# Kernel tuning notes

Hardware: AMD Instinct MI355X
Metric: run time of the kernel (lower is better)

The kernel has to match this reference:

```python
import jax, jax.numpy as jnp
import numpy as np

B, N, K, CIN, COUT = 2, 8192, 16, 64, 64


def setup_inputs() -> dict:
    key = jax.random.key(0)
    ks = jax.random.split(key, 12)
    w = lambda k, shape: jax.random.normal(k, shape, jnp.float32) * 0.02
    return dict(
        pos=jax.random.normal(ks[0], (B, N, 3), jnp.float32),
        features=jax.random.normal(ks[1], (B, N, CIN), jnp.float32),
        emb_w=w(ks[2], (CIN, COUT)), emb_b=jnp.zeros((COUT,), jnp.float32),
        wq=w(ks[3], (COUT, COUT)), wk=w(ks[4], (COUT, COUT)), wv=w(ks[5], (COUT, COUT)),
        pe_w1=w(ks[6], (3, COUT)), pe_b1=jnp.zeros((COUT,), jnp.float32),
        pe_w2=w(ks[7], (COUT, COUT)), pe_b2=jnp.zeros((COUT,), jnp.float32),
        at_w1=w(ks[8], (COUT, COUT)), at_b1=jnp.zeros((COUT,), jnp.float32),
        at_w2=w(ks[9], (COUT, COUT)), at_b2=jnp.zeros((COUT,), jnp.float32),
        out_w=w(ks[10], (COUT, CIN)), out_b=jnp.zeros((CIN,), jnp.float32),
    )


def _gather(x, idx):
    # x: [B, N, C], idx: [B, N, K] -> [B, N, K, C]
    return jax.vmap(lambda xb, ib: xb[ib])(x, idx)


def reference(pos, features, emb_w, emb_b, wq, wk, wv,
              pe_w1, pe_b1, pe_w2, pe_b2,
              at_w1, at_b1, at_w2, at_b2, out_w, out_b):
    # KNN: squared pairwise distances, take k smallest (includes self)
    sq = jnp.sum(pos * pos, axis=-1)                                  # [B, N]
    d2 = sq[:, :, None] + sq[:, None, :] - 2.0 * jnp.einsum('bnd,bmd->bnm', pos, pos)
    _, knn_idx = jax.lax.top_k(-d2, K)                                # [B, N, K]

    # recenter_groups: neighbor positions relative to query point
    grouped_pos = _gather(pos, knn_idx) - pos[:, :, None, :]          # [B, N, K, 3]

    x = features @ emb_w + emb_b                                      # [B, N, COUT]
    q = x @ wq                                                        # [B, N, COUT]
    k = _gather(x @ wk, knn_idx)                                      # [B, N, K, COUT]
    v = _gather(x @ wv, knn_idx)                                      # [B, N, K, COUT]

    # mlp_posenc: Linear(3,C) -> ReLU -> Linear(C,C)
    posenc = jax.nn.relu(grouped_pos @ pe_w1 + pe_b1) @ pe_w2 + pe_b2  # [B, N, K, COUT]

    # mlp_attn on (q - k + posenc), softmax over neighbor axis (dim=-2)
    h = q[:, :, None, :] - k + posenc
    attn = jax.nn.relu(h @ at_w1 + at_b1) @ at_w2 + at_b2
    attn = jax.nn.softmax(attn / np.float32(np.sqrt(COUT)), axis=-2)

    result = jnp.einsum('bmnf,bmnf->bmf', attn, v + posenc)           # [B, N, COUT]
    return result @ out_w + out_b + features                          # [B, N, CIN]
```

## Files before the change

### kernel.cpp

```cpp
#include <hip/hip_runtime.h>
#include <hip/hip_bf16.h>

#define BB 2
#define NN 8192
#define SPL 16
#define CAND (NN/SPL)
#define NPTS (BB*NN)

#define POS4_OFF 0u
#define WBUF_OFF 65536u
#define PART_OFF 99328u
#define QB_OFF   99328u
#define KVB_OFF  (QB_OFF + 1048576u)
#define IDX_OFF  4293632u
#define WT_OFF   (IDX_OFF + 262144u)

#define W_EMB 0
#define W_Q   4096
#define W_K   8192
#define W_V   12288
#define W_PE2 16384
#define W_AT1 20480
#define W_AT2 24576
#define W_OUT 28672
#define W_PE1 32768
#define B_EMB 32960
#define B_PE1 33024
#define B_PE2 33088
#define B_AT1 33152
#define B_AT2 33216
#define B_OUT 33280

typedef __attribute__((ext_vector_type(8))) short bf16x8;
typedef __attribute__((ext_vector_type(4))) float f32x4;

__device__ __forceinline__ unsigned umn(unsigned a, unsigned b) {
#if __has_builtin(__builtin_elementwise_min)
  return __builtin_elementwise_min(a, b);
#else
  return a < b ? a : b;
#endif
}
__device__ __forceinline__ unsigned umx(unsigned a, unsigned b) {
#if __has_builtin(__builtin_elementwise_max)
  return __builtin_elementwise_max(a, b);
#else
  return a < b ? b : a;
#endif
}

__device__ inline unsigned short f2bf(float x) {
  __hip_bfloat16 b = __float2bfloat16(x);
  return *(unsigned short*)&b;
}

#define HCOL(c, j) ((((((c) >> 3) + (j)) & 7) << 3) | ((c) & 7))

__global__ __launch_bounds__(256) void k0_stage(
    const float* __restrict__ pos,
    const float* __restrict__ emb_w, const float* __restrict__ emb_b,
    const float* __restrict__ wq, const float* __restrict__ wk,
    const float* __restrict__ wv,
    const float* __restrict__ pe_w1, const float* __restrict__ pe_b1,
    const float* __restrict__ pe_w2, const float* __restrict__ pe_b2,
    const float* __restrict__ at_w1, const float* __restrict__ at_b1,
    const float* __restrict__ at_w2, const float* __restrict__ at_b2,
    const float* __restrict__ out_w, const float* __restrict__ out_b,
    float* __restrict__ ws)
{
  int t = blockIdx.x * 256 + threadIdx.x;
  if (t < NPTS) {
    float x = pos[t * 3 + 0], y = pos[t * 3 + 1], z = pos[t * 3 + 2];
    float* o = ws + POS4_OFF + t * 4;
    o[0] = x; o[1] = y; o[2] = z;
    o[3] = fmaf(x, x, fmaf(y, y, z * z));
    return;
  }
  t -= NPTS;
  float* wbuf = ws + WBUF_OFF;
  if (t < 32768) {
    const float* s;
    switch (t >> 12) {
      case 0: s = emb_w; break;
      case 1: s = wq;    break;
      case 2: s = wk;    break;
      case 3: s = wv;    break;
      case 4: s = pe_w2; break;
      case 5: s = at_w1; break;
      case 6: s = at_w2; break;
      default: s = out_w; break;
    }
    wbuf[t] = s[t & 4095];
    return;
  }
  t -= 32768;
  if (t < 192) { wbuf[W_PE1 + t] = pe_w1[t]; return; }
  t -= 192;
  if (t < 384) {
    const float* s;
    switch (t >> 6) {
      case 0: s = emb_b; break;
      case 1: s = pe_b1; break;
      case 2: s = pe_b2; break;
      case 3: s = at_b1; break;
      case 4: s = at_b2; break;
      default: s = out_b; break;
    }
    wbuf[B_EMB + t] = s[t & 63];
    return;
  }
  t -= 384;
  if (t < 16384) {
    unsigned short* wt = (unsigned short*)(ws + WT_OFF);
    const float* s;
    switch (t >> 12) {
      case 0: s = pe_w2; break;
      case 1: s = at_w1; break;
      case 2: s = at_w2; break;
      default: s = out_w; break;
    }
    int idx = t & 4095, f = idx >> 6, c = idx & 63;
    wt[t] = f2bf(s[c * 64 + f]);
  }
}

__global__ __launch_bounds__(256) void k1_knn(const float* __restrict__ pos4,
                                              unsigned* __restrict__ part)
{
  const int tid = threadIdx.x;
  const int g = blockIdx.x * 256 + tid;
  const int s = blockIdx.y;
  const int bu = __builtin_amdgcn_readfirstlane(g >> 13);
  const float4* __restrict__ allp = (const float4*)pos4;
  const float4 q = allp[g];
  const float qx2 = -2.f * q.x, qy2 = -2.f * q.y, qz2 = -2.f * q.z;
  const float sqq = q.w + 1e-5f;
  const float4* __restrict__ cand = allp + (bu * NN + s * CAND);
  unsigned m[16];
#pragma unroll
  for (int i = 0; i < 16; i++) m[i] = 0xFFFFFFFFu;
  const unsigned jb = (unsigned)(s * CAND);

  constexpr int OE[63][2] = {
    {0,1},{2,3},{4,5},{6,7},{8,9},{10,11},{12,13},{14,15},
    {0,2},{1,3},{4,6},{5,7},{8,10},{9,11},{12,14},{13,15},
    {1,2},{5,6},{9,10},{13,14},
    {0,4},{1,5},{2,6},{3,7},{8,12},{9,13},{10,14},{11,15},
    {2,4},{3,5},{10,12},{11,13},
    {1,2},{3,4},{5,6},{9,10},{11,12},{13,14},
    {0,8},{1,9},{2,10},{3,11},{4,12},{5,13},{6,14},{7,15},
    {4,8},{5,9},{6,10},{7,11},
    {2,4},{3,5},{6,8},{7,9},{10,12},{11,13},
    {1,2},{3,4},{5,6},{7,8},{9,10},{11,12},{13,14}
  };

  for (int j0 = 0; j0 < CAND; j0 += 16) {
    unsigned b[16];
#pragma unroll
    for (int i = 0; i < 16; i++) {
      float4 cp = cand[j0 + i];
      float d2 = fmaf(cp.x, qx2, fmaf(cp.y, qy2, fmaf(cp.z, qz2, cp.w + sqq)));
      b[i] = (__float_as_uint(d2) & 0xFFFFE000u) | (jb + (unsigned)(j0 + i));
    }
#pragma unroll
    for (int c = 0; c < 63; c++) {
      const int x = OE[c][0], y = OE[c][1];
      unsigned lo = umn(b[x], b[y]);
      unsigned hi = umx(b[x], b[y]);
      b[x] = hi; b[y] = lo;
    }
#pragma unroll
    for (int i = 0; i < 16; i++) m[i] = umn(m[i], b[i]);
#pragma unroll
    for (int d = 8; d; d >>= 1) {
#pragma unroll
      for (int i = 0; i < 16; i++) {
        if ((i & d) == 0) {
          const int l = i | d;
          unsigned lo = umn(m[i], m[l]);
          unsigned hi = umx(m[i], m[l]);
          m[i] = lo; m[l] = hi;
        }
      }
    }
  }
#pragma unroll
  for (int i = 0; i < 16; i++)
    part[(unsigned)(s * 16 + i) * NPTS + (unsigned)g] = m[i];
}

__global__ __launch_bounds__(256) void k2_merge(const unsigned* __restrict__ part,
                                                int* __restrict__ knn_idx)
{
  const int g = blockIdx.x * 256 + threadIdx.x;
  unsigned run[16];
#pragma unroll
  for (int i = 0; i < 16; i++) run[i] = part[i * NPTS + g];
#pragma unroll
  for (int l = 1; l < SPL; l++) {
#pragma unroll
    for (int i = 0; i < 16; i++)
      run[i] = umn(run[i], part[(l * 16 + 15 - i) * NPTS + g]);
#pragma unroll
    for (int d = 8; d; d >>= 1) {
#pragma unroll
      for (int i = 0; i < 16; i++) {
        if ((i & d) == 0) {
          const int l2 = i | d;
          unsigned lo = umn(run[i], run[l2]);
          unsigned hi = umx(run[i], run[l2]);
          run[i] = lo; run[l2] = hi;
        }
      }
    }
  }
  const int base = (g >> 13) * NN;
  int outv[16];
#pragma unroll
  for (int i = 0; i < 16; i++) outv[i] = base + (int)(run[i] & 0x1FFFu);
  int4* o = (int4*)(knn_idx + g * 16);
  o[0] = make_int4(outv[0], outv[1], outv[2], outv[3]);
  o[1] = make_int4(outv[4], outv[5], outv[6], outv[7]);
  o[2] = make_int4(outv[8], outv[9], outv[10], outv[11]);
  o[3] = make_int4(outv[12], outv[13], outv[14], outv[15]);
}

__global__ __launch_bounds__(256) void k34_embqkv(
    const float* __restrict__ feat, const float* __restrict__ wb,
    float* __restrict__ qo, unsigned* __restrict__ kvp)
{
  __shared__ float wl[16384];
  __shared__ float xl[2048];
  for (int i = threadIdx.x; i < 16384; i += 256) wl[i] = wb[W_EMB + i];
  const int col = threadIdx.x & 63;
  const int rg = threadIdx.x >> 6;
  const int row0 = blockIdx.x * 32 + rg * 8;
  const int rowu = __builtin_amdgcn_readfirstlane(row0);
  __syncthreads();
  {
    float acc[8];
    float bias = wb[B_EMB + col];
#pragma unroll
    for (int r = 0; r < 8; r++) acc[r] = bias;
    for (int c = 0; c < 64; c++) {
      float w = wl[c * 64 + col];
      const float* fp = feat + rowu * 64 + c;
#pragma unroll
      for (int r = 0; r < 8; r++) acc[r] = fmaf(fp[r * 64], w, acc[r]);
    }
#pragma unroll
    for (int r = 0; r < 8; r++) xl[(rg * 8 + r) * 64 + col] = acc[r];
  }
  __syncthreads();
  float aq[8], ak[8], av[8];
#pragma unroll
  for (int r = 0; r < 8; r++) { aq[r] = 0.f; ak[r] = 0.f; av[r] = 0.f; }
  for (int c = 0; c < 64; c++) {
    float w0 = wl[4096 + c * 64 + col];
    float w1 = wl[8192 + c * 64 + col];
    float w2 = wl[12288 + c * 64 + col];
#pragma unroll
    for (int r = 0; r < 8; r++) {
      float xv = xl[(rg * 8 + r) * 64 + c];
      aq[r] = fmaf(xv, w0, aq[r]);
      ak[r] = fmaf(xv, w1, ak[r]);
      av[r] = fmaf(xv, w2, av[r]);
    }
  }
#pragma unroll
  for (int r = 0; r < 8; r++) {
    qo[(row0 + r) * 64 + col] = aq[r];
    kvp[(row0 + r) * 64 + col] =
        ((unsigned)f2bf(av[r]) << 16) | (unsigned)f2bf(ak[r]);
  }
}

__device__ inline void mv(const unsigned short* hm, const bf16x8 B[4][2],
                          const float bias[4], int ln, int s0, int s1,
                          f32x4 acc[4])
{
  bf16x8 a0 = *(const bf16x8*)(hm + ln * 64 + s0);
  bf16x8 a1 = *(const bf16x8*)(hm + ln * 64 + s1);
#pragma unroll
  for (int t = 0; t < 4; t++) {
    f32x4 a = {bias[t], bias[t], bias[t], bias[t]};
    a = __builtin_amdgcn_mfma_f32_16x16x32_bf16(a0, B[t][0], a, 0, 0, 0);
    a = __builtin_amdgcn_mfma_f32_16x16x32_bf16(a1, B[t][1], a, 0, 0, 0);
    acc[t] = a;
  }
}

__global__ __launch_bounds__(256, 2) void k5_attn(
    const float* __restrict__ pos4, const float* __restrict__ qg,
    const unsigned* __restrict__ kvp, const float* __restrict__ featf,
    const float* __restrict__ wb, const unsigned short* __restrict__ wt,
    const int* __restrict__ knn, float* __restrict__ out)
{
  __shared__ unsigned short hma[4][1024];
  __shared__ unsigned short resm[1024];
  const int tid = threadIdx.x;
  const int wid = tid >> 6, lane = tid & 63;
  const int ln = lane & 15, quad = lane >> 4;
  unsigned short* hm = hma[wid];
  const int s0 = ((quad + ln) & 7) << 3;
  const int s1 = ((4 + quad + ln) & 7) << 3;

  bf16x8 Bf[3][4][2];
#pragma unroll
  for (int m = 0; m < 3; m++)
#pragma unroll
    for (int t = 0; t < 4; t++)
#pragma unroll
      for (int ks = 0; ks < 2; ks++)
        Bf[m][t][ks] = *(const bf16x8*)(wt + m * 4096 + (t * 16 + ln) * 64 +
                                        ks * 32 + quad * 8);
  bf16x8 bo[2];
#pragma unroll
  for (int ks = 0; ks < 2; ks++)
    bo[ks] = *(const bf16x8*)(wt + 3 * 4096 + (wid * 16 + ln) * 64 +
                              ks * 32 + quad * 8);

  float pw10 = wb[W_PE1 + lane], pw11 = wb[W_PE1 + 64 + lane],
        pw12 = wb[W_PE1 + 128 + lane];
  float pb1 = wb[B_PE1 + lane];
  float bpe[4], ba1[4], ba2[4];
#pragma unroll
  for (int t = 0; t < 4; t++) {
    bpe[t] = wb[B_PE2 + t * 16 + ln];
    ba1[t] = wb[B_AT1 + t * 16 + ln];
    ba2[t] = wb[B_AT2 + t * 16 + ln];
  }

  const int p0 = blockIdx.x * 16 + wid * 4;
  const int ps0 = __builtin_amdgcn_readfirstlane(p0);
  int4 cur[4];
  {
    const int4* ip4 = (const int4*)(knn + ps0 * 16);
#pragma unroll
    for (int u = 0; u < 4; u++) cur[u] = ip4[u];
  }

  for (int pp = 0; pp < 4; pp++) {
    const int p = p0 + pp;
    const int ps = __builtin_amdgcn_readfirstlane(p);
    int jj[16];
#pragma unroll
    for (int u = 0; u < 4; u++) {
      jj[u*4+0] = cur[u].x; jj[u*4+1] = cur[u].y;
      jj[u*4+2] = cur[u].z; jj[u*4+3] = cur[u].w;
    }
    int4 nxt[4];
    {
      const int pn = (pp < 3) ? (ps + 1) : ps;
      const int4* np4 = (const int4*)(knn + pn * 16);
#pragma unroll
      for (int u = 0; u < 4; u++) nxt[u] = np4[u];
    }
    unsigned kvw[4][4];
#pragma unroll
    for (int r = 0; r < 4; r++) {
      const unsigned* kp = kvp + jj[quad * 4 + r] * 64 + ln;
#pragma unroll
      for (int t = 0; t < 4; t++) kvw[r][t] = kp[t * 16];
    }
    float qv[4];
#pragma unroll
    for (int t = 0; t < 4; t++) qv[t] = qg[p * 64 + t * 16 + ln];

    const float* mp = pos4 + ps * 4;
    float pnx = mp[0], pny = mp[1], pnz = mp[2];
#pragma unroll
    for (int j = 0; j < 16; j++) {
      const float* np_ = pos4 + jj[j] * 4;
      float h1 = fmaf(np_[2] - pnz, pw12,
                 fmaf(np_[1] - pny, pw11,
                 fmaf(np_[0] - pnx, pw10, pb1)));
      hm[j * 64 + HCOL(lane, j)] = f2bf(fmaxf(h1, 0.f));
    }
    f32x4 accp[4];
    mv(hm, Bf[0], bpe, ln, s0, s1, accp);
    float vpe[4][4];
#pragma unroll
    for (int r = 0; r < 4; r++) {
      const int j = quad * 4 + r;
#pragma unroll
      for (int t = 0; t < 4; t++) {
        const unsigned w = kvw[r][t];
        float kf = __uint_as_float(w << 16);
        float vf = __uint_as_float(w & 0xFFFF0000u);
        float pe = accp[t][r];
        vpe[t][r] = vf + pe;
        hm[j * 64 + HCOL(t * 16 + ln, j)] = f2bf(qv[t] - kf + pe);
      }
    }
    f32x4 acch[4];
    mv(hm, Bf[1], ba1, ln, s0, s1, acch);
#pragma unroll
    for (int t = 0; t < 4; t++)
#pragma unroll
      for (int r = 0; r < 4; r++) {
        const int j = quad * 4 + r;
        hm[j * 64 + HCOL(t * 16 + ln, j)] = f2bf(fmaxf(acch[t][r], 0.f));
      }
    f32x4 lg[4];
    mv(hm, Bf[2], ba2, ln, s0, s1, lg);
    const int pb = wid * 4 + pp;
#pragma unroll
    for (int t = 0; t < 4; t++) {
      float e0 = __expf(lg[t][0] * 0.125f);
      float e1 = __expf(lg[t][1] * 0.125f);
      float e2 = __expf(lg[t][2] * 0.125f);
      float e3 = __expf(lg[t][3] * 0.125f);
      float ss = (e0 + e1) + (e2 + e3);
      float dt = fmaf(e3, vpe[t][3], fmaf(e2, vpe[t][2],
                 fmaf(e1, vpe[t][1], e0 * vpe[t][0])));
      ss += __shfl_xor(ss, 16); ss += __shfl_xor(ss, 32);
      dt += __shfl_xor(dt, 16); dt += __shfl_xor(dt, 32);
      float res = dt / ss;
      if (quad == 0) resm[pb * 64 + HCOL(t * 16 + ln, pb)] = f2bf(res);
    }
#pragma unroll
    for (int u = 0; u < 4; u++) cur[u] = nxt[u];
  }
  __syncthreads();
  {
    const int nt = wid;
    float ob = wb[B_OUT + nt * 16 + ln];
    f32x4 acc = {ob, ob, ob, ob};
#pragma unroll
    for (int ks = 0; ks < 2; ks++) {
      bf16x8 a = *(const bf16x8*)(resm + ln * 64 +
                                  (((ks * 4 + quad + ln) & 7) << 3));
      acc = __builtin_amdgcn_mfma_f32_16x16x32_bf16(a, bo[ks], acc, 0, 0, 0);
    }
#pragma unroll
    for (int r = 0; r < 4; r++) {
      const int pt = blockIdx.x * 16 + quad * 4 + r;
      const int f = nt * 16 + ln;
      out[pt * 64 + f] = acc[r] + featf[pt * 64 + f];
    }
  }
}

extern "C" void kernel_launch(void* const* d_in, const int* in_sizes, int n_in,
                              void* d_out, int out_size, void* d_ws, size_t ws_size,
                              hipStream_t stream)
{
  (void)in_sizes; (void)n_in; (void)out_size; (void)ws_size;
  const float* pos   = (const float*)d_in[0];
  const float* feat  = (const float*)d_in[1];
  const float* emb_w = (const float*)d_in[2];
  const float* emb_b = (const float*)d_in[3];
  const float* wq    = (const float*)d_in[4];
  const float* wk    = (const float*)d_in[5];
  const float* wv    = (const float*)d_in[6];
  const float* pe_w1 = (const float*)d_in[7];
  const float* pe_b1 = (const float*)d_in[8];
  const float* pe_w2 = (const float*)d_in[9];
  const float* pe_b2 = (const float*)d_in[10];
  const float* at_w1 = (const float*)d_in[11];
  const float* at_b1 = (const float*)d_in[12];
  const float* at_w2 = (const float*)d_in[13];
  const float* at_b2 = (const float*)d_in[14];
  const float* out_w = (const float*)d_in[15];
  const float* out_b = (const float*)d_in[16];
  float* ws = (float*)d_ws;

  k0_stage<<<259, 256, 0, stream>>>(pos, emb_w, emb_b, wq, wk, wv,
      pe_w1, pe_b1, pe_w2, pe_b2, at_w1, at_b1, at_w2, at_b2, out_w, out_b, ws);
  dim3 g1(NPTS / 256, SPL);
  k1_knn<<<g1, 256, 0, stream>>>(ws + POS4_OFF, (unsigned*)ws + PART_OFF);
  k2_merge<<<NPTS / 256, 256, 0, stream>>>((unsigned*)ws + PART_OFF,
                                           (int*)ws + IDX_OFF);
  k34_embqkv<<<NPTS / 32, 256, 0, stream>>>(feat, ws + WBUF_OFF,
                                            ws + QB_OFF, (unsigned*)ws + KVB_OFF);
  k5_attn<<<NPTS / 16, 256, 0, stream>>>(ws + POS4_OFF, ws + QB_OFF,
      (unsigned*)ws + KVB_OFF, feat, ws + WBUF_OFF,
      (unsigned short*)(ws + WT_OFF), (int*)ws + IDX_OFF, (float*)d_out);
}
```

Before: 236.9 us.

## Drop staging kernel, read raw inputs directly, and use 8-wide KNN batches

Removes the k0_stage kernel. Positions, weights and biases are now read directly from the input tensors, and the bf16 transposed-weight conversion is folded into extra blocks of the merge kernel. The KNN inner loop now loads raw xyz triples, computes the exact difference-based distance, and sorts 8 candidates per step with a 19-comparator network before merging into the bottom half of the running top-16. This saves a launch and a staging pass, but adds more merge steps per candidate and unaligned 3-float loads in the KNN and attention gathers.

```diff
diff --git a/kernel.cpp b/kernel.cpp
--- a/kernel.cpp
+++ b/kernel.cpp
@@ -7,29 +7,11 @@
 #define CAND (NN/SPL)
 #define NPTS (BB*NN)
 
-#define POS4_OFF 0u
-#define WBUF_OFF 65536u
-#define PART_OFF 99328u
-#define QB_OFF   99328u
-#define KVB_OFF  (QB_OFF + 1048576u)
-#define IDX_OFF  4293632u
-#define WT_OFF   (IDX_OFF + 262144u)
-
-#define W_EMB 0
-#define W_Q   4096
-#define W_K   8192
-#define W_V   12288
-#define W_PE2 16384
-#define W_AT1 20480
-#define W_AT2 24576
-#define W_OUT 28672
-#define W_PE1 32768
-#define B_EMB 32960
-#define B_PE1 33024
-#define B_PE2 33088
-#define B_AT1 33152
-#define B_AT2 33216
-#define B_OUT 33280
+#define PART_OFF 0u
+#define IDX_OFF  4194304u
+#define WT_OFF   4456448u
+#define QB_OFF   0u
+#define KVB_OFF  1048576u
 
 typedef __attribute__((ext_vector_type(8))) short bf16x8;
 typedef __attribute__((ext_vector_type(4))) float f32x4;
@@ -56,121 +38,51 @@
 
 #define HCOL(c, j) ((((((c) >> 3) + (j)) & 7) << 3) | ((c) & 7))
 
-__global__ __launch_bounds__(256) void k0_stage(
-    const float* __restrict__ pos,
-    const float* __restrict__ emb_w, const float* __restrict__ emb_b,
-    const float* __restrict__ wq, const float* __restrict__ wk,
-    const float* __restrict__ wv,
-    const float* __restrict__ pe_w1, const float* __restrict__ pe_b1,
-    const float* __restrict__ pe_w2, const float* __restrict__ pe_b2,
-    const float* __restrict__ at_w1, const float* __restrict__ at_b1,
-    const float* __restrict__ at_w2, const float* __restrict__ at_b2,
-    const float* __restrict__ out_w, const float* __restrict__ out_b,
-    float* __restrict__ ws)
-{
-  int t = blockIdx.x * 256 + threadIdx.x;
-  if (t < NPTS) {
-    float x = pos[t * 3 + 0], y = pos[t * 3 + 1], z = pos[t * 3 + 2];
-    float* o = ws + POS4_OFF + t * 4;
-    o[0] = x; o[1] = y; o[2] = z;
-    o[3] = fmaf(x, x, fmaf(y, y, z * z));
-    return;
-  }
-  t -= NPTS;
-  float* wbuf = ws + WBUF_OFF;
-  if (t < 32768) {
-    const float* s;
-    switch (t >> 12) {
-      case 0: s = emb_w; break;
-      case 1: s = wq;    break;
-      case 2: s = wk;    break;
-      case 3: s = wv;    break;
-      case 4: s = pe_w2; break;
-      case 5: s = at_w1; break;
-      case 6: s = at_w2; break;
-      default: s = out_w; break;
-    }
-    wbuf[t] = s[t & 4095];
-    return;
-  }
-  t -= 32768;
-  if (t < 192) { wbuf[W_PE1 + t] = pe_w1[t]; return; }
-  t -= 192;
-  if (t < 384) {
-    const float* s;
-    switch (t >> 6) {
-      case 0: s = emb_b; break;
-      case 1: s = pe_b1; break;
-      case 2: s = pe_b2; break;
-      case 3: s = at_b1; break;
-      case 4: s = at_b2; break;
-      default: s = out_b; break;
-    }
-    wbuf[B_EMB + t] = s[t & 63];
-    return;
-  }
-  t -= 384;
-  if (t < 16384) {
-    unsigned short* wt = (unsigned short*)(ws + WT_OFF);
-    const float* s;
-    switch (t >> 12) {
-      case 0: s = pe_w2; break;
-      case 1: s = at_w1; break;
-      case 2: s = at_w2; break;
-      default: s = out_w; break;
-    }
-    int idx = t & 4095, f = idx >> 6, c = idx & 63;
-    wt[t] = f2bf(s[c * 64 + f]);
-  }
-}
-
-__global__ __launch_bounds__(256) void k1_knn(const float* __restrict__ pos4,
+__global__ __launch_bounds__(256) void k1_knn(const float* __restrict__ pos,
                                               unsigned* __restrict__ part)
 {
   const int tid = threadIdx.x;
   const int g = blockIdx.x * 256 + tid;
   const int s = blockIdx.y;
   const int bu = __builtin_amdgcn_readfirstlane(g >> 13);
-  const float4* __restrict__ allp = (const float4*)pos4;
-  const float4 q = allp[g];
-  const float qx2 = -2.f * q.x, qy2 = -2.f * q.y, qz2 = -2.f * q.z;
-  const float sqq = q.w + 1e-5f;
-  const float4* __restrict__ cand = allp + (bu * NN + s * CAND);
+  const float qx = pos[g * 3 + 0], qy = pos[g * 3 + 1], qz = pos[g * 3 + 2];
+  const float* __restrict__ cp = pos + (bu * NN + s * CAND) * 3;
+  const unsigned jb = (unsigned)(s * CAND);
   unsigned m[16];
 #pragma unroll
   for (int i = 0; i < 16; i++) m[i] = 0xFFFFFFFFu;
-  const unsigned jb = (unsigned)(s * CAND);
-
-  constexpr int OE[63][2] = {
-    {0,1},{2,3},{4,5},{6,7},{8,9},{10,11},{12,13},{14,15},
-    {0,2},{1,3},{4,6},{5,7},{8,10},{9,11},{12,14},{13,15},
-    {1,2},{5,6},{9,10},{13,14},
-    {0,4},{1,5},{2,6},{3,7},{8,12},{9,13},{10,14},{11,15},
-    {2,4},{3,5},{10,12},{11,13},
-    {1,2},{3,4},{5,6},{9,10},{11,12},{13,14},
-    {0,8},{1,9},{2,10},{3,11},{4,12},{5,13},{6,14},{7,15},
-    {4,8},{5,9},{6,10},{7,11},
-    {2,4},{3,5},{6,8},{7,9},{10,12},{11,13},
-    {1,2},{3,4},{5,6},{7,8},{9,10},{11,12},{13,14}
+
+  constexpr int OE8[19][2] = {
+    {0,1},{2,3},{4,5},{6,7},
+    {0,2},{1,3},{4,6},{5,7},
+    {1,2},{5,6},
+    {0,4},{1,5},{2,6},{3,7},
+    {2,4},{3,5},
+    {1,2},{3,4},{5,6}
   };
 
-  for (int j0 = 0; j0 < CAND; j0 += 16) {
-    unsigned b[16];
-#pragma unroll
-    for (int i = 0; i < 16; i++) {
-      float4 cp = cand[j0 + i];
-      float d2 = fmaf(cp.x, qx2, fmaf(cp.y, qy2, fmaf(cp.z, qz2, cp.w + sqq)));
+  for (int j0 = 0; j0 < CAND; j0 += 8) {
+    float c[24];
+#pragma unroll
+    for (int i = 0; i < 24; i++) c[i] = cp[j0 * 3 + i];
+    unsigned b[8];
+#pragma unroll
+    for (int i = 0; i < 8; i++) {
+      float dx = c[i * 3 + 0] - qx;
+      float dy = c[i * 3 + 1] - qy;
+      float dz = c[i * 3 + 2] - qz;
+      float d2 = fmaf(dx, dx, fmaf(dy, dy, dz * dz));
       b[i] = (__float_as_uint(d2) & 0xFFFFE000u) | (jb + (unsigned)(j0 + i));
     }
 #pragma unroll
-    for (int c = 0; c < 63; c++) {
-      const int x = OE[c][0], y = OE[c][1];
+    for (int cc = 0; cc < 19; cc++) {
+      const int x = OE8[cc][0], y = OE8[cc][1];
       unsigned lo = umn(b[x], b[y]);
       unsigned hi = umx(b[x], b[y]);
       b[x] = hi; b[y] = lo;
     }
 #pragma unroll
-    for (int i = 0; i < 16; i++) m[i] = umn(m[i], b[i]);
+    for (int i = 0; i < 8; i++) m[8 + i] = umn(m[8 + i], b[i]);
 #pragma unroll
     for (int d = 8; d; d >>= 1) {
 #pragma unroll
@@ -189,9 +101,25 @@
     part[(unsigned)(s * 16 + i) * NPTS + (unsigned)g] = m[i];
 }
 
-__global__ __launch_bounds__(256) void k2_merge(const unsigned* __restrict__ part,
-                                                int* __restrict__ knn_idx)
-{
+__global__ __launch_bounds__(256) void k2_merge(
+    const unsigned* __restrict__ part, int* __restrict__ knn_idx,
+    const float* __restrict__ pe_w2, const float* __restrict__ at_w1,
+    const float* __restrict__ at_w2, const float* __restrict__ out_w,
+    unsigned short* __restrict__ wt)
+{
+  if (blockIdx.x >= 64) {
+    const int t = (blockIdx.x - 64) * 256 + threadIdx.x;
+    const float* s;
+    switch (t >> 12) {
+      case 0: s = pe_w2; break;
+      case 1: s = at_w1; break;
+      case 2: s = at_w2; break;
+      default: s = out_w; break;
+    }
+    const int idx = t & 4095, f = idx >> 6, c = idx & 63;
+    wt[t] = f2bf(s[c * 64 + f]);
+    return;
+  }
   const int g = blockIdx.x * 256 + threadIdx.x;
   unsigned run[16];
 #pragma unroll
@@ -226,12 +154,20 @@
 }
 
 __global__ __launch_bounds__(256) void k34_embqkv(
-    const float* __restrict__ feat, const float* __restrict__ wb,
+    const float* __restrict__ feat,
+    const float* __restrict__ emb_w, const float* __restrict__ emb_b,
+    const float* __restrict__ wq, const float* __restrict__ wk,
+    const float* __restrict__ wv,
     float* __restrict__ qo, unsigned* __restrict__ kvp)
 {
   __shared__ float wl[16384];
   __shared__ float xl[2048];
-  for (int i = threadIdx.x; i < 16384; i += 256) wl[i] = wb[W_EMB + i];
+  for (int i = threadIdx.x; i < 4096; i += 256) {
+    wl[i] = emb_w[i];
+    wl[4096 + i] = wq[i];
+    wl[8192 + i] = wk[i];
+    wl[12288 + i] = wv[i];
+  }
   const int col = threadIdx.x & 63;
   const int rg = threadIdx.x >> 6;
   const int row0 = blockIdx.x * 32 + rg * 8;
@@ -239,7 +175,7 @@
   __syncthreads();
   {
     float acc[8];
-    float bias = wb[B_EMB + col];
+    float bias = emb_b[col];
 #pragma unroll
     for (int r = 0; r < 8; r++) acc[r] = bias;
     for (int c = 0; c < 64; c++) {
@@ -291,10 +227,13 @@
 }
 
 __global__ __launch_bounds__(256, 2) void k5_attn(
-    const float* __restrict__ pos4, const float* __restrict__ qg,
+    const float* __restrict__ pos, const float* __restrict__ qg,
     const unsigned* __restrict__ kvp, const float* __restrict__ featf,
-    const float* __restrict__ wb, const unsigned short* __restrict__ wt,
-    const int* __restrict__ knn, float* __restrict__ out)
+    const float* __restrict__ pe_w1, const float* __restrict__ pe_b1,
+    const float* __restrict__ pe_b2, const float* __restrict__ at_b1,
+    const float* __restrict__ at_b2, const float* __restrict__ out_b,
+    const unsigned short* __restrict__ wt, const int* __restrict__ knn,
+    float* __restrict__ out)
 {
   __shared__ unsigned short hma[4][1024];
   __shared__ unsigned short resm[1024];
@@ -320,15 +259,14 @@
     bo[ks] = *(const bf16x8*)(wt + 3 * 4096 + (wid * 16 + ln) * 64 +
                               ks * 32 + quad * 8);
 
-  float pw10 = wb[W_PE1 + lane], pw11 = wb[W_PE1 + 64 + lane],
-        pw12 = wb[W_PE1 + 128 + lane];
-  float pb1 = wb[B_PE1 + lane];
+  float pw10 = pe_w1[lane], pw11 = pe_w1[64 + lane], pw12 = pe_w1[128 + lane];
+  float pb1 = pe_b1[lane];
   float bpe[4], ba1[4], ba2[4];
 #pragma unroll
   for (int t = 0; t < 4; t++) {
-    bpe[t] = wb[B_PE2 + t * 16 + ln];
-    ba1[t] = wb[B_AT1 + t * 16 + ln];
-    ba2[t] = wb[B_AT2 + t * 16 + ln];
+    bpe[t] = pe_b2[t * 16 + ln];
+    ba1[t] = at_b1[t * 16 + ln];
+    ba2[t] = at_b2[t * 16 + ln];
   }
 
   const int p0 = blockIdx.x * 16 + wid * 4;
@@ -367,11 +305,11 @@
 #pragma unroll
     for (int t = 0; t < 4; t++) qv[t] = qg[p * 64 + t * 16 + ln];
 
-    const float* mp = pos4 + ps * 4;
+    const float* mp = pos + ps * 3;
     float pnx = mp[0], pny = mp[1], pnz = mp[2];
 #pragma unroll
     for (int j = 0; j < 16; j++) {
-      const float* np_ = pos4 + jj[j] * 4;
+      const float* np_ = pos + jj[j] * 3;
       float h1 = fmaf(np_[2] - pnz, pw12,
                  fmaf(np_[1] - pny, pw11,
                  fmaf(np_[0] - pnx, pw10, pb1)));
@@ -425,7 +363,7 @@
   __syncthreads();
   {
     const int nt = wid;
-    float ob = wb[B_OUT + nt * 16 + ln];
+    float ob = out_b[nt * 16 + ln];
     f32x4 acc = {ob, ob, ob, ob};
 #pragma unroll
     for (int ks = 0; ks < 2; ks++) {
@@ -466,15 +404,14 @@
   const float* out_b = (const float*)d_in[16];
   float* ws = (float*)d_ws;
 
-  k0_stage<<<259, 256, 0, stream>>>(pos, emb_w, emb_b, wq, wk, wv,
-      pe_w1, pe_b1, pe_w2, pe_b2, at_w1, at_b1, at_w2, at_b2, out_w, out_b, ws);
   dim3 g1(NPTS / 256, SPL);
-  k1_knn<<<g1, 256, 0, stream>>>(ws + POS4_OFF, (unsigned*)ws + PART_OFF);
-  k2_merge<<<NPTS / 256, 256, 0, stream>>>((unsigned*)ws + PART_OFF,
-                                           (int*)ws + IDX_OFF);
-  k34_embqkv<<<NPTS / 32, 256, 0, stream>>>(feat, ws + WBUF_OFF,
-                                            ws + QB_OFF, (unsigned*)ws + KVB_OFF);
-  k5_attn<<<NPTS / 16, 256, 0, stream>>>(ws + POS4_OFF, ws + QB_OFF,
-      (unsigned*)ws + KVB_OFF, feat, ws + WBUF_OFF,
+  k1_knn<<<g1, 256, 0, stream>>>(pos, (unsigned*)ws + PART_OFF);
+  k2_merge<<<128, 256, 0, stream>>>((unsigned*)ws + PART_OFF,
+      (int*)ws + IDX_OFF, pe_w2, at_w1, at_w2, out_w,
+      (unsigned short*)(ws + WT_OFF));
+  k34_embqkv<<<NPTS / 32, 256, 0, stream>>>(feat, emb_w, emb_b, wq, wk, wv,
+      ws + QB_OFF, (unsigned*)ws + KVB_OFF);
+  k5_attn<<<NPTS / 16, 256, 0, stream>>>(pos, ws + QB_OFF,
+      (unsigned*)ws + KVB_OFF, feat, pe_w1, pe_b1, pe_b2, at_b1, at_b2, out_b,
       (unsigned short*)(ws + WT_OFF), (int*)ws + IDX_OFF, (float*)d_out);
 }
```

Result: no change. 240.1 us (+1.4%).
